# Kernel tuning notes

Measured on AMD Instinct MI355X. Metric: run time of the kernel, lower is better.

Reference implementation:

```python
import jax, jax.numpy as jnp
import numpy as np

B, T, C, DU, OUT = 16, 2048, 1024, 1024, 512
CIF_THRESHOLD = 1.0


def setup_inputs():
    key = jax.random.key(0)
    k0, k1, k2, k3, k4, k5 = jax.random.split(key, 6)
    encoder_out = jax.random.normal(k0, (B, T, C), dtype=jnp.float32)
    input_lengths = (T // 2 + jax.random.randint(k1, (B,), 0, T // 2)).astype(jnp.int32)
    target_lengths = (200 + jax.random.randint(k2, (B,), 0, 300)).astype(jnp.int32)
    s = 1.0 / np.sqrt(C)
    Wd = jax.random.uniform(k3, (DU, C), jnp.float32, -s, s)
    bd = jnp.zeros((DU,), jnp.float32)
    sp = 1.0 / np.sqrt(DU)
    Wp = jax.random.uniform(k4, (1, DU), jnp.float32, -sp, sp)
    bp = jnp.zeros((1,), jnp.float32)
    Wo = jax.random.uniform(k5, (OUT, C), jnp.float32, -s, s)
    return {"encoder_out": encoder_out, "input_lengths": input_lengths,
            "target_lengths": target_lengths, "Wd": Wd, "bd": bd,
            "Wp": Wp, "bp": bp, "Wo": Wo}


def _cif_forward(encoder_out, input_lengths, target_lengths, Wd, bd, Wp, bp, Wo):
    Bsz, Tlen, Cdim = encoder_out.shape
    pos = jnp.arange(Tlen)
    not_pad = (pos[None, :] < input_lengths[:, None]).astype(encoder_out.dtype)  # [B,T]

    # dense weight production: relu(x Wd^T + bd) -> sigmoid(. Wp^T + bp)
    h = jax.nn.relu(jnp.einsum('btc,dc->btd', encoder_out, Wd) + bd)
    weight = jax.nn.sigmoid(jnp.einsum('btd,od->bto', h, Wp)[..., 0] + bp[0])
    org_weight = weight * not_pad

    # training-time scaling so weights sum to target_lengths
    scale = target_lengths.astype(encoder_out.dtype) / (org_weight.sum(-1) + 1e-8)
    weight = org_weight * scale[:, None]

    padding_start_id = input_lengths  # = not_padding_mask.sum(-1)

    def step(carry, xs):
        acc_w, acc_s = carry                     # [B], [B,C]
        w, e, i = xs                             # [B], [B,C], scalar step idx
        fired = (acc_w + w) >= CIF_THRESHOLD     # [B]
        remained = 1.0 - acc_w
        new_w = jnp.where(fired, w - remained, w + acc_w)
        new_s = jnp.where(fired[:, None], (w - remained)[:, None] * e,
                          acc_s + w[:, None] * e)
        f_s = jnp.where(fired[:, None], acc_s + remained[:, None] * e, 0.0)
        f_s = jnp.where((i > padding_start_id)[:, None], 0.0, f_s)
        return (new_w, new_s), f_s

    init = (jnp.zeros((Bsz,), encoder_out.dtype),
            jnp.zeros((Bsz, Cdim), encoder_out.dtype))
    _, fired_states = jax.lax.scan(
        step, init,
        (weight.T, jnp.transpose(encoder_out, (1, 0, 2)), jnp.arange(Tlen)))
    fired_states = jnp.transpose(fired_states, (1, 0, 2))  # [B,T,C]

    fired_marks = jnp.abs(fired_states).sum(-1) != 0.0     # [B,T]
    # stable-compact fired frames to front; pad to T (upper bound of fired_max_length)
    order = jnp.argsort(jnp.logical_not(fired_marks).astype(jnp.int32), axis=1)
    n_fired = fired_marks.sum(-1)                           # [B]
    valid = pos[None, :] < n_fired[:, None]                 # [B,T]
    cif_outputs = jnp.take_along_axis(fired_states, order[:, :, None], axis=1)
    cif_outputs = cif_outputs * valid[:, :, None].astype(cif_outputs.dtype)

    idx = jnp.where(valid, order, 0).astype(jnp.int32)
    prev = jnp.concatenate([jnp.zeros((Bsz, 1), jnp.int32), idx[:, :-1]], axis=1)
    cif_durations = (idx - prev) * valid.astype(jnp.int32)

    base_mask = (pos[None, :] == 0).astype(jnp.int32)       # [1,0,0,...] fallback
    cif_out_padding_mask = jnp.where((n_fired > 0)[:, None],
                                     valid.astype(jnp.int32), base_mask)
    quantity_out = org_weight.sum(-1)                       # training branch
    cif_outputs = jnp.einsum('btc,oc->bto', cif_outputs, Wo)  # bias-free output proj
    return cif_outputs, cif_out_padding_mask, cif_durations, quantity_out


def reference(encoder_out, input_lengths, target_lengths, Wd, bd, Wp, bp, Wo):
    return _cif_forward(encoder_out, input_lengths, target_lengths,
                        Wd, bd, Wp, bp, Wo)
```

## Files before the change

kernel.cpp:

```cpp
#include <hip/hip_runtime.h>
#include <cstdint>
#include <cstddef>

#define BSZ 16
#define TLEN 2048
#define CDIM 1024
#define OUTDIM 512
#define MAXF 512

typedef _Float16 f16x8 __attribute__((ext_vector_type(8)));
typedef _Float16 f16x4 __attribute__((ext_vector_type(4)));
typedef float f32x16 __attribute__((ext_vector_type(16)));

__device__ __forceinline__ void gl_lds16(const void* g, void* l) {
    __builtin_amdgcn_global_load_lds(
        (const __attribute__((address_space(1))) void*)g,
        (__attribute__((address_space(3))) void*)l, 16, 0, 0);
}

struct h2pair { _Float16 h0, h1; };
__device__ __forceinline__ h2pair split2(float a) {
    h2pair o;
    o.h0 = (_Float16)a;
    float r = a - (float)o.h0;
    o.h1 = (_Float16)(r * 2048.0f);
    return o;
}

__global__ __launch_bounds__(128) void k0a_split_wd(
    const float* __restrict__ Wd, _Float16* __restrict__ B0,
    _Float16* __restrict__ B1)
{
    const int dut = blockIdx.x;
    const int ktl = blockIdx.y;
    const int r = threadIdx.x;
    const float* src = Wd + (size_t)(dut * 128 + r) * CDIM + ktl * 32;
    float v[32];
#pragma unroll
    for (int j = 0; j < 8; j++) *(float4*)&v[j * 4] = *(const float4*)(src + j * 4);
    const size_t tb = (size_t)(dut * 32 + ktl) * 4096;
#pragma unroll
    for (int c = 0; c < 4; c++) {
        f16x8 h0, h1;
#pragma unroll
        for (int j = 0; j < 8; j++) {
            h2pair s = split2(v[c * 8 + j]);
            h0[j] = s.h0;
            h1[j] = s.h1;
        }
        *(f16x8*)&B0[tb + (c * 128 + r) * 8] = h0;
        *(f16x8*)&B1[tb + (c * 128 + r) * 8] = h1;
    }
}

__global__ __launch_bounds__(256) void k0c_split_wo(
    const float* __restrict__ Wo, _Float16* __restrict__ W0,
    _Float16* __restrict__ W1)
{
    const int i = (blockIdx.x * 256 + threadIdx.x) * 4;
    float4 v = *(const float4*)(Wo + i);
    f16x4 h0, h1;
    h2pair s0 = split2(v.x); h0[0] = s0.h0; h1[0] = s0.h1;
    h2pair s1 = split2(v.y); h0[1] = s1.h0; h1[1] = s1.h1;
    h2pair s2 = split2(v.z); h0[2] = s2.h0; h1[2] = s2.h1;
    h2pair s3 = split2(v.w); h0[3] = s3.h0; h1[3] = s3.h1;
    *(f16x4*)&W0[i] = h0;
    *(f16x4*)&W1[i] = h1;
}

__global__ __launch_bounds__(256, 2) void k1_weight_gemm(
    const float* __restrict__ enc, const _Float16* __restrict__ BT0,
    const _Float16* __restrict__ BT1, const float* __restrict__ bd,
    const float* __restrict__ Wp, float* __restrict__ g)
{
    __shared__ __align__(16) _Float16 lds[32768];

    const int tid = threadIdx.x;
    const int lane = tid & 63;
    const int wv = tid >> 6;
    const int l5 = lane & 31;
    const int hi = lane >> 5;
    const int mtb = (wv & 1) * 64;
    const int ntb = (wv >> 1) * 64;

    const int bx = blockIdx.x;
    const int xcd = bx & 7;
    const int j = bx >> 3;
    const int rg = xcd * 32 + (j >> 3);
    const int du = j & 7;
    const long row0 = (long)rg * 128;
    const int du0 = du * 128;

    const int sr = tid >> 1;
    const int sh = tid & 1;
    const float* aptr = enc + (row0 + sr) * (long)CDIM + sh * 16;

    const _Float16* btile = ((wv >> 1) ? BT1 : BT0) + (size_t)du * 32 * 4096;
    const int bh = wv & 1;
    const int bofs = 8192 + (wv >> 1) * 4096 + bh * 2048;

    f32x16 acc[2][2], accc[2][2];
#pragma unroll
    for (int mt = 0; mt < 2; mt++)
#pragma unroll
        for (int nt = 0; nt < 2; nt++)
#pragma unroll
            for (int r = 0; r < 16; r++) { acc[mt][nt][r] = 0.f; accc[mt][nt][r] = 0.f; }

    float fa[16];

#pragma unroll
    for (int jj = 0; jj < 4; jj++)
        *(float4*)&fa[jj * 4] = *(const float4*)(aptr + jj * 4);
    {
        f16x8 va0[2], va1[2];
#pragma unroll
        for (int c = 0; c < 2; c++)
#pragma unroll
            for (int jj = 0; jj < 8; jj++) {
                h2pair s = split2(fa[c * 8 + jj]);
                va0[c][jj] = s.h0;
                va1[c][jj] = s.h1;
            }
#pragma unroll
        for (int c = 0; c < 2; c++) {
            *(f16x8*)&lds[((sh * 2 + c) * 128 + sr) * 8] = va0[c];
            *(f16x8*)&lds[4096 + ((sh * 2 + c) * 128 + sr) * 8] = va1[c];
        }
#pragma unroll
        for (int c = 0; c < 4; c++)
            gl_lds16(btile + (bh * 256 + c * 64 + lane) * 8,
                     &lds[bofs + c * 512]);
    }
#pragma unroll
    for (int jj = 0; jj < 4; jj++)
        *(float4*)&fa[jj * 4] = *(const float4*)(aptr + 32 + jj * 4);

    for (int kt = 0; kt < 32; ++kt) {
        const int cur = (kt & 1) * 16384;
        const int nxt = ((kt & 1) ^ 1) * 16384;

        __syncthreads();

        if (kt < 31) {
#pragma unroll
            for (int c = 0; c < 4; c++)
                gl_lds16(btile + (size_t)(kt + 1) * 4096 + (bh * 256 + c * 64 + lane) * 8,
                         &lds[nxt + bofs + c * 512]);
            f16x8 va0[2], va1[2];
#pragma unroll
            for (int c = 0; c < 2; c++)
#pragma unroll
                for (int jj = 0; jj < 8; jj++) {
                    h2pair s = split2(fa[c * 8 + jj]);
                    va0[c][jj] = s.h0;
                    va1[c][jj] = s.h1;
                }
#pragma unroll
            for (int c = 0; c < 2; c++) {
                *(f16x8*)&lds[nxt + ((sh * 2 + c) * 128 + sr) * 8] = va0[c];
                *(f16x8*)&lds[nxt + 4096 + ((sh * 2 + c) * 128 + sr) * 8] = va1[c];
            }
            if (kt < 30) {
#pragma unroll
                for (int jj = 0; jj < 4; jj++)
                    *(float4*)&fa[jj * 4] = *(const float4*)(aptr + (kt + 2) * 32 + jj * 4);
            }
        }

#pragma unroll
        for (int ks = 0; ks < 2; ks++) {
            const int ch = ks * 2 + hi;
            f16x8 A0[2], A1[2], B0[2], B1[2];
#pragma unroll
            for (int mt = 0; mt < 2; mt++) {
                const int row = mtb + mt * 32 + l5;
                A0[mt] = *(const f16x8*)&lds[cur + (ch * 128 + row) * 8];
                A1[mt] = *(const f16x8*)&lds[cur + 4096 + (ch * 128 + row) * 8];
            }
#pragma unroll
            for (int nt = 0; nt < 2; nt++) {
                const int row = ntb + nt * 32 + l5;
                B0[nt] = *(const f16x8*)&lds[cur + 8192 + (ch * 128 + row) * 8];
                B1[nt] = *(const f16x8*)&lds[cur + 12288 + (ch * 128 + row) * 8];
            }
#pragma unroll
            for (int mt = 0; mt < 2; mt++)
#pragma unroll
                for (int nt = 0; nt < 2; nt++) {
                    acc[mt][nt] = __builtin_amdgcn_mfma_f32_32x32x16_f16(
                        A0[mt], B0[nt], acc[mt][nt], 0, 0, 0);
                    accc[mt][nt] = __builtin_amdgcn_mfma_f32_32x32x16_f16(
                        A0[mt], B1[nt], accc[mt][nt], 0, 0, 0);
                    accc[mt][nt] = __builtin_amdgcn_mfma_f32_32x32x16_f16(
                        A1[mt], B0[nt], accc[mt][nt], 0, 0, 0);
                }
        }
    }

    float bdv[2], wpv[2];
#pragma unroll
    for (int nt = 0; nt < 2; nt++) {
        int n = du0 + ntb + nt * 32 + l5;
        bdv[nt] = bd[n];
        wpv[nt] = Wp[n];
    }
    float pm[2][16];
#pragma unroll
    for (int mt = 0; mt < 2; mt++)
#pragma unroll
        for (int r = 0; r < 16; r++) {
            float s = 0.f;
#pragma unroll
            for (int nt = 0; nt < 2; nt++) {
                float h = acc[mt][nt][r] + 4.8828125e-4f * accc[mt][nt][r] + bdv[nt];
                h = h > 0.f ? h : 0.f;
                s += wpv[nt] * h;
            }
            s += __shfl_xor(s, 1);
            s += __shfl_xor(s, 2);
            s += __shfl_xor(s, 4);
            s += __shfl_xor(s, 8);
            s += __shfl_xor(s, 16);
            pm[mt][r] = s;
        }
    float out = 0.f;
#pragma unroll
    for (int mt = 0; mt < 2; mt++)
#pragma unroll
        for (int r = 0; r < 16; r++)
            if (l5 == mt * 16 + r) out = pm[mt][r];
    const int mt_sel = l5 >> 4;
    const int r_sel = l5 & 15;
    const int row = mtb + mt_sel * 32 + (r_sel & 3) + 8 * (r_sel >> 2) + 4 * hi;
    atomicAdd(&g[row0 + row], out);
}

__global__ __launch_bounds__(256) void k2_scan(
    const float* __restrict__ g, const int* __restrict__ in_len,
    const int* __restrict__ tgt_len, const float* __restrict__ bp,
    float* __restrict__ c_a, float* __restrict__ c_b,
    int* __restrict__ fire_t, int* __restrict__ n_fired,
    float* __restrict__ out_mask, float* __restrict__ out_dur,
    float* __restrict__ out_qty)
{
    __shared__ float w[TLEN];
    __shared__ float ca[TLEN];
    __shared__ float cb[TLEN];
    __shared__ int fires[MAXF];
    __shared__ float ssum[256];
    __shared__ float s_scale;
    __shared__ int s_nf;

    const int b = blockIdx.x;
    const int tid = threadIdx.x;
    const int len = in_len[b];
    const float bpv = bp[0];

    float local = 0.f;
    for (int t = tid; t < TLEN; t += 256) {
        float gv = g[b * TLEN + t] + bpv;
        float s = 1.f / (1.f + expf(-gv));
        float ow = (t < len) ? s : 0.f;
        w[t] = ow;
        local += ow;
    }
    ssum[tid] = local;
    __syncthreads();
    for (int st = 128; st > 0; st >>= 1) {
        if (tid < st) ssum[tid] += ssum[tid + st];
        __syncthreads();
    }
    if (tid == 0) {
        float org_sum = ssum[0];
        out_qty[b] = org_sum;
        s_scale = (float)tgt_len[b] / (org_sum + 1e-8f);
    }
    __syncthreads();
    float scale = s_scale;
    for (int t = tid; t < TLEN; t += 256) w[t] *= scale;
    __syncthreads();

    if (tid == 0) {
        float accw = 0.f;
        int k = 0;
        int t = 0;
        for (; t + 8 <= len; t += 8) {
            float4 wa = *(const float4*)&w[t];
            float4 wb4 = *(const float4*)&w[t + 4];
            float wv8[8] = {wa.x, wa.y, wa.z, wa.w, wb4.x, wb4.y, wb4.z, wb4.w};
#pragma unroll
            for (int u = 0; u < 8; u++) {
                float wt = wv8[u];
                float aw = accw + wt;
                bool f = (aw >= 1.0f);
                float rem = 1.0f - accw;
                float fb = wt - rem;
                ca[t + u] = f ? rem : wt;
                cb[t + u] = f ? fb : 0.f;
                fires[k & (MAXF - 1)] = t + u;
                k += f ? 1 : 0;
                accw = f ? fb : aw;
            }
        }
        for (; t < len; t++) {
            float wt = w[t];
            float aw = accw + wt;
            bool f = (aw >= 1.0f);
            float rem = 1.0f - accw;
            float fb = wt - rem;
            ca[t] = f ? rem : wt;
            cb[t] = f ? fb : 0.f;
            fires[k & (MAXF - 1)] = t;
            k += f ? 1 : 0;
            accw = f ? fb : aw;
        }
        s_nf = (k < MAXF) ? k : MAXF;
        n_fired[b] = s_nf;
    }
    __syncthreads();

    for (int t = tid; t < len; t += 256) {
        c_a[b * TLEN + t] = ca[t];
        c_b[b * TLEN + t] = cb[t];
    }
    const int nf = s_nf;
    for (int jj = tid; jj < nf; jj += 256) {
        int tj = fires[jj];
        fire_t[b * MAXF + jj] = tj;
        out_mask[b * TLEN + jj] = 1.0f;
        int prev = (jj == 0) ? 0 : fires[jj - 1];
        out_dur[b * TLEN + jj] = (float)(tj - prev);
    }
    if (tid == 0 && nf == 0) out_mask[b * TLEN] = 1.0f;
}

__global__ __launch_bounds__(256) void k3a_compact(
    const float* __restrict__ enc, const float* __restrict__ c_a,
    const float* __restrict__ c_b, const int* __restrict__ fire_t,
    const int* __restrict__ n_fired, _Float16* __restrict__ C0,
    _Float16* __restrict__ C1)
{
    const int b = blockIdx.y;
    const int k = blockIdx.x;
    const int tid = threadIdx.x;
    _Float16* d0 = C0 + ((size_t)b * MAXF + k) * CDIM + tid * 4;
    _Float16* d1 = C1 + ((size_t)b * MAXF + k) * CDIM + tid * 4;
    if (k >= n_fired[b]) {
        f16x4 z = {(_Float16)0.f, (_Float16)0.f, (_Float16)0.f, (_Float16)0.f};
        *(f16x4*)d0 = z;
        *(f16x4*)d1 = z;
        return;
    }
    const int tend = fire_t[b * MAXF + k];
    const int tprev = (k == 0) ? -1 : fire_t[b * MAXF + k - 1];
    float ax = 0.f, ay = 0.f, az = 0.f, aw = 0.f;
    const int tstart = (tprev < 0) ? 0 : tprev;
    for (int t = tstart; t <= tend; t++) {
        float coef = (t == tprev) ? c_b[b * TLEN + t] : c_a[b * TLEN + t];
        const float4 e = *(const float4*)(enc + ((size_t)b * TLEN + t) * CDIM + tid * 4);
        ax += coef * e.x;
        ay += coef * e.y;
        az += coef * e.z;
        aw += coef * e.w;
    }
    f16x4 h0, h1;
    h2pair s0 = split2(ax); h0[0] = s0.h0; h1[0] = s0.h1;
    h2pair s1 = split2(ay); h0[1] = s1.h0; h1[1] = s1.h1;
    h2pair s2 = split2(az); h0[2] = s2.h0; h1[2] = s2.h1;
    h2pair s3 = split2(aw); h0[3] = s3.h0; h1[3] = s3.h1;
    *(f16x4*)d0 = h0;
    *(f16x4*)d1 = h1;
}

__global__ __launch_bounds__(256, 2) void k3b_outproj(
    const _Float16* __restrict__ C0, const _Float16* __restrict__ C1,
    const _Float16* __restrict__ W0, const _Float16* __restrict__ W1,
    const int* __restrict__ n_fired, float* __restrict__ out0)
{
    __shared__ __align__(16) _Float16 lds[16384];

    const int b = blockIdx.z;
    const int nf = n_fired[b];
    const int j0 = blockIdx.x * 128;
    if (j0 >= nf) return;
    const int o0 = blockIdx.y * 128;
    const int tid = threadIdx.x;
    const int lane = tid & 63;
    const int wv = tid >> 6;
    const int l5 = lane & 31;
    const int hi = lane >> 5;
    const int mtb = (wv & 1) * 64;
    const int ntb = (wv >> 1) * 64;

    const int sr = tid >> 1;
    const int sh = tid & 1;
    const _Float16* a0p = C0 + ((size_t)b * MAXF + j0 + sr) * CDIM + sh * 16;
    const _Float16* a1p = C1 + ((size_t)b * MAXF + j0 + sr) * CDIM + sh * 16;
    const _Float16* b0p = W0 + (size_t)(o0 + sr) * CDIM + sh * 16;
    const _Float16* b1p = W1 + (size_t)(o0 + sr) * CDIM + sh * 16;

    f32x16 acc[2][2], accc[2][2];
#pragma unroll
    for (int mt = 0; mt < 2; mt++)
#pragma unroll
        for (int nt = 0; nt < 2; nt++)
#pragma unroll
            for (int r = 0; r < 16; r++) { acc[mt][nt][r] = 0.f; accc[mt][nt][r] = 0.f; }

    f16x8 xa0[2], xa1[2], xb0[2], xb1[2];
#pragma unroll
    for (int c = 0; c < 2; c++) {
        xa0[c] = *(const f16x8*)(a0p + c * 8);
        xa1[c] = *(const f16x8*)(a1p + c * 8);
        xb0[c] = *(const f16x8*)(b0p + c * 8);
        xb1[c] = *(const f16x8*)(b1p + c * 8);
    }

    for (int kt = 0; kt < 32; ++kt) {
        __syncthreads();
#pragma unroll
        for (int c = 0; c < 2; c++) {
            *(f16x8*)&lds[((sh * 2 + c) * 128 + sr) * 8] = xa0[c];
            *(f16x8*)&lds[4096 + ((sh * 2 + c) * 128 + sr) * 8] = xa1[c];
            *(f16x8*)&lds[8192 + ((sh * 2 + c) * 128 + sr) * 8] = xb0[c];
            *(f16x8*)&lds[12288 + ((sh * 2 + c) * 128 + sr) * 8] = xb1[c];
        }
        __syncthreads();
        if (kt < 31) {
            const int o = (kt + 1) * 32;
#pragma unroll
            for (int c = 0; c < 2; c++) {
                xa0[c] = *(const f16x8*)(a0p + o + c * 8);
                xa1[c] = *(const f16x8*)(a1p + o + c * 8);
                xb0[c] = *(const f16x8*)(b0p + o + c * 8);
                xb1[c] = *(const f16x8*)(b1p + o + c * 8);
            }
        }
#pragma unroll
        for (int ks = 0; ks < 2; ks++) {
            const int ch = ks * 2 + hi;
            f16x8 A0[2], A1[2], B0[2], B1[2];
#pragma unroll
            for (int mt = 0; mt < 2; mt++) {
                const int row = mtb + mt * 32 + l5;
                A0[mt] = *(const f16x8*)&lds[(ch * 128 + row) * 8];
                A1[mt] = *(const f16x8*)&lds[4096 + (ch * 128 + row) * 8];
            }
#pragma unroll
            for (int nt = 0; nt < 2; nt++) {
                const int row = ntb + nt * 32 + l5;
                B0[nt] = *(const f16x8*)&lds[8192 + (ch * 128 + row) * 8];
                B1[nt] = *(const f16x8*)&lds[12288 + (ch * 128 + row) * 8];
            }
#pragma unroll
            for (int mt = 0; mt < 2; mt++)
#pragma unroll
                for (int nt = 0; nt < 2; nt++) {
                    acc[mt][nt] = __builtin_amdgcn_mfma_f32_32x32x16_f16(
                        A0[mt], B0[nt], acc[mt][nt], 0, 0, 0);
                    accc[mt][nt] = __builtin_amdgcn_mfma_f32_32x32x16_f16(
                        A0[mt], B1[nt], accc[mt][nt], 0, 0, 0);
                    accc[mt][nt] = __builtin_amdgcn_mfma_f32_32x32x16_f16(
                        A1[mt], B0[nt], accc[mt][nt], 0, 0, 0);
                }
        }
    }

#pragma unroll
    for (int mt = 0; mt < 2; mt++)
#pragma unroll
        for (int nt = 0; nt < 2; nt++)
#pragma unroll
            for (int r = 0; r < 16; r++) {
                float val = acc[mt][nt][r] + 4.8828125e-4f * accc[mt][nt][r];
                int m = mtb + mt * 32 + (r & 3) + 8 * (r >> 2) + 4 * hi;
                int col = o0 + ntb + nt * 32 + l5;
                out0[((size_t)b * TLEN + j0 + m) * OUTDIM + col] = val;
            }
}

extern "C" void kernel_launch(void* const* d_in, const int* in_sizes, int n_in,
                              void* d_out, int out_size, void* d_ws, size_t ws_size,
                              hipStream_t stream)
{
    const float* enc = (const float*)d_in[0];
    const int* in_len = (const int*)d_in[1];
    const int* tgt_len = (const int*)d_in[2];
    const float* Wd = (const float*)d_in[3];
    const float* bd = (const float*)d_in[4];
    const float* Wp = (const float*)d_in[5];
    const float* bp = (const float*)d_in[6];
    const float* Wo = (const float*)d_in[7];

    char* ws = (char*)d_ws;
    float* g       = (float*)(ws + 0);
    float* c_a     = (float*)(ws + 131072);
    float* c_b     = (float*)(ws + 262144);
    int* fire_t    = (int*)(ws + 393216);
    int* n_fired   = (int*)(ws + 425984);
    _Float16* WdT0 = (_Float16*)(ws + 458752);
    _Float16* WdT1 = (_Float16*)(ws + 2555904);
    _Float16* Wo0  = (_Float16*)(ws + 4653056);
    _Float16* Wo1  = (_Float16*)(ws + 5701632);
    _Float16* C0   = (_Float16*)(ws + 6750208);
    _Float16* C1   = (_Float16*)(ws + 23527424);

    float* out0 = (float*)d_out;
    float* out_mask = out0 + (size_t)BSZ * TLEN * OUTDIM;
    float* out_dur = out_mask + (size_t)BSZ * TLEN;
    float* out_qty = out_dur + (size_t)BSZ * TLEN;

    (void)hipMemsetAsync(g, 0, 131072, stream);
    (void)hipMemsetAsync(d_out, 0, (size_t)out_size * 4, stream);

    k0a_split_wd<<<dim3(8, 32), 128, 0, stream>>>(Wd, WdT0, WdT1);
    k0c_split_wo<<<512, 256, 0, stream>>>(Wo, Wo0, Wo1);
    k1_weight_gemm<<<2048, 256, 0, stream>>>(enc, WdT0, WdT1, bd, Wp, g);
    k2_scan<<<BSZ, 256, 0, stream>>>(g, in_len, tgt_len, bp, c_a, c_b,
                                     fire_t, n_fired, out_mask, out_dur, out_qty);
    k3a_compact<<<dim3(MAXF, BSZ), 256, 0, stream>>>(enc, c_a, c_b, fire_t,
                                                     n_fired, C0, C1);
    k3b_outproj<<<dim3(4, 4, BSZ), 256, 0, stream>>>(C0, C1, Wo0, Wo1,
                                                     n_fired, out0);
}
```

Baseline: 591.6 us.

## Interleave A-tile split/store between MFMA halves with manual waitcnt barriers

Restructures the main K loop of the dense-weight GEMM. The fp32-to-split-fp16 conversion and LDS store of the next A tile now sit between the two k-substep MFMA groups, so VALU and LDS work overlaps matrix math. The __syncthreads at loop top is replaced by one end-of-iteration s_barrier preceded by explicit s_waitcnt vmcnt(4)/lgkmcnt(0), which lets the next iteration's A prefetch global loads stay in flight. s_setprio raises wave priority around MFMA blocks. The hand-written waitcnt counts depend on exact instruction ordering and could race if the compiler reorders loads.

```diff
diff --git a/kernel.cpp b/kernel.cpp
--- a/kernel.cpp
+++ b/kernel.cpp
@@ -132,45 +132,27 @@
             gl_lds16(btile + (bh * 256 + c * 64 + lane) * 8,
                      &lds[bofs + c * 512]);
     }
+    asm volatile("" ::: "memory");
 #pragma unroll
     for (int jj = 0; jj < 4; jj++)
         *(float4*)&fa[jj * 4] = *(const float4*)(aptr + 32 + jj * 4);
+    asm volatile("s_waitcnt vmcnt(4) lgkmcnt(0)" ::: "memory");
+    __builtin_amdgcn_s_barrier();
 
     for (int kt = 0; kt < 32; ++kt) {
         const int cur = (kt & 1) * 16384;
-        const int nxt = ((kt & 1) ^ 1) * 16384;
-
-        __syncthreads();
+        const int nxt = cur ^ 16384;
 
         if (kt < 31) {
 #pragma unroll
             for (int c = 0; c < 4; c++)
                 gl_lds16(btile + (size_t)(kt + 1) * 4096 + (bh * 256 + c * 64 + lane) * 8,
                          &lds[nxt + bofs + c * 512]);
-            f16x8 va0[2], va1[2];
-#pragma unroll
-            for (int c = 0; c < 2; c++)
-#pragma unroll
-                for (int jj = 0; jj < 8; jj++) {
-                    h2pair s = split2(fa[c * 8 + jj]);
-                    va0[c][jj] = s.h0;
-                    va1[c][jj] = s.h1;
-                }
-#pragma unroll
-            for (int c = 0; c < 2; c++) {
-                *(f16x8*)&lds[nxt + ((sh * 2 + c) * 128 + sr) * 8] = va0[c];
-                *(f16x8*)&lds[nxt + 4096 + ((sh * 2 + c) * 128 + sr) * 8] = va1[c];
-            }
-            if (kt < 30) {
-#pragma unroll
-                for (int jj = 0; jj < 4; jj++)
-                    *(float4*)&fa[jj * 4] = *(const float4*)(aptr + (kt + 2) * 32 + jj * 4);
-            }
-        }
-
-#pragma unroll
-        for (int ks = 0; ks < 2; ks++) {
-            const int ch = ks * 2 + hi;
+        }
+        asm volatile("" ::: "memory");
+
+        {
+            const int ch = hi;
             f16x8 A0[2], A1[2], B0[2], B1[2];
 #pragma unroll
             for (int mt = 0; mt < 2; mt++) {
@@ -184,6 +166,7 @@
                 B0[nt] = *(const f16x8*)&lds[cur + 8192 + (ch * 128 + row) * 8];
                 B1[nt] = *(const f16x8*)&lds[cur + 12288 + (ch * 128 + row) * 8];
             }
+            __builtin_amdgcn_s_setprio(1);
 #pragma unroll
             for (int mt = 0; mt < 2; mt++)
 #pragma unroll
@@ -195,6 +178,70 @@
                     accc[mt][nt] = __builtin_amdgcn_mfma_f32_32x32x16_f16(
                         A1[mt], B0[nt], accc[mt][nt], 0, 0, 0);
                 }
+            __builtin_amdgcn_s_setprio(0);
+        }
+
+        f16x8 A0b[2], A1b[2], B0b[2], B1b[2];
+        {
+            const int ch = 2 + hi;
+#pragma unroll
+            for (int mt = 0; mt < 2; mt++) {
+                const int row = mtb + mt * 32 + l5;
+                A0b[mt] = *(const f16x8*)&lds[cur + (ch * 128 + row) * 8];
+                A1b[mt] = *(const f16x8*)&lds[cur + 4096 + (ch * 128 + row) * 8];
+            }
+#pragma unroll
+            for (int nt = 0; nt < 2; nt++) {
+                const int row = ntb + nt * 32 + l5;
+                B0b[nt] = *(const f16x8*)&lds[cur + 8192 + (ch * 128 + row) * 8];
+                B1b[nt] = *(const f16x8*)&lds[cur + 12288 + (ch * 128 + row) * 8];
+            }
+        }
+
+        if (kt < 31) {
+            f16x8 va0[2], va1[2];
+#pragma unroll
+            for (int c = 0; c < 2; c++)
+#pragma unroll
+                for (int jj = 0; jj < 8; jj++) {
+                    h2pair s = split2(fa[c * 8 + jj]);
+                    va0[c][jj] = s.h0;
+                    va1[c][jj] = s.h1;
+                }
+#pragma unroll
+            for (int c = 0; c < 2; c++) {
+                *(f16x8*)&lds[nxt + ((sh * 2 + c) * 128 + sr) * 8] = va0[c];
+                *(f16x8*)&lds[nxt + 4096 + ((sh * 2 + c) * 128 + sr) * 8] = va1[c];
+            }
+            if (kt < 30) {
+#pragma unroll
+                for (int jj = 0; jj < 4; jj++)
+                    *(float4*)&fa[jj * 4] = *(const float4*)(aptr + (kt + 2) * 32 + jj * 4);
+            }
+        }
+
+        {
+            __builtin_amdgcn_s_setprio(1);
+#pragma unroll
+            for (int mt = 0; mt < 2; mt++)
+#pragma unroll
+                for (int nt = 0; nt < 2; nt++) {
+                    acc[mt][nt] = __builtin_amdgcn_mfma_f32_32x32x16_f16(
+                        A0b[mt], B0b[nt], acc[mt][nt], 0, 0, 0);
+                    accc[mt][nt] = __builtin_amdgcn_mfma_f32_32x32x16_f16(
+                        A0b[mt], B1b[nt], accc[mt][nt], 0, 0, 0);
+                    accc[mt][nt] = __builtin_amdgcn_mfma_f32_32x32x16_f16(
+                        A1b[mt], B0b[nt], accc[mt][nt], 0, 0, 0);
+                }
+            __builtin_amdgcn_s_setprio(0);
+        }
+
+        if (kt < 31) {
+            if (kt < 30)
+                asm volatile("s_waitcnt vmcnt(4) lgkmcnt(0)" ::: "memory");
+            else
+                asm volatile("s_waitcnt vmcnt(0) lgkmcnt(0)" ::: "memory");
+            __builtin_amdgcn_s_barrier();
         }
     }
 
```

Measured after the change: 605.0 us. 2.3% more time.

## Pre-split encoder into fp16 tiles and stream both operands via async LDS loads

Applied to the files above, without the earlier changes.

Adds a separate pass that splits the fp32 encoder into hi/lo fp16 tiled buffers. The weight GEMM then loads both A and B tiles with global_load_lds instead of converting A in registers each k-step. The block grows to 512 threads (8 waves, 32-wide N per wave) and MFMA sections are wrapped in setprio. This removes per-iteration split work and register staging from the GEMM loop, but adds a full extra read/write pass over the 128MB encoder (writing 128MB of fp16 halves), which may cost more than it saves. E0 reuses the C0 workspace region, which relies on ordering with later kernels.

```diff
diff --git a/kernel.cpp b/kernel.cpp
--- a/kernel.cpp
+++ b/kernel.cpp
@@ -27,18 +27,18 @@
     return o;
 }
 
-__global__ __launch_bounds__(128) void k0a_split_wd(
-    const float* __restrict__ Wd, _Float16* __restrict__ B0,
-    _Float16* __restrict__ B1)
-{
-    const int dut = blockIdx.x;
+__global__ __launch_bounds__(128) void k0_split_tiled(
+    const float* __restrict__ src_, _Float16* __restrict__ P0,
+    _Float16* __restrict__ P1)
+{
+    const int rgp = blockIdx.x;
     const int ktl = blockIdx.y;
     const int r = threadIdx.x;
-    const float* src = Wd + (size_t)(dut * 128 + r) * CDIM + ktl * 32;
+    const float* src = src_ + (size_t)(rgp * 128 + r) * CDIM + ktl * 32;
     float v[32];
 #pragma unroll
     for (int j = 0; j < 8; j++) *(float4*)&v[j * 4] = *(const float4*)(src + j * 4);
-    const size_t tb = (size_t)(dut * 32 + ktl) * 4096;
+    const size_t tb = (size_t)(rgp * 32 + ktl) * 4096;
 #pragma unroll
     for (int c = 0; c < 4; c++) {
         f16x8 h0, h1;
@@ -48,8 +48,8 @@
             h0[j] = s.h0;
             h1[j] = s.h1;
         }
-        *(f16x8*)&B0[tb + (c * 128 + r) * 8] = h0;
-        *(f16x8*)&B1[tb + (c * 128 + r) * 8] = h1;
+        *(f16x8*)&P0[tb + (c * 128 + r) * 8] = h0;
+        *(f16x8*)&P1[tb + (c * 128 + r) * 8] = h1;
     }
 }
 
@@ -68,10 +68,11 @@
     *(f16x4*)&W1[i] = h1;
 }
 
-__global__ __launch_bounds__(256, 2) void k1_weight_gemm(
-    const float* __restrict__ enc, const _Float16* __restrict__ BT0,
-    const _Float16* __restrict__ BT1, const float* __restrict__ bd,
-    const float* __restrict__ Wp, float* __restrict__ g)
+__global__ __launch_bounds__(512, 4) void k1_weight_gemm(
+    const _Float16* __restrict__ E0, const _Float16* __restrict__ E1,
+    const _Float16* __restrict__ BT0, const _Float16* __restrict__ BT1,
+    const float* __restrict__ bd, const float* __restrict__ Wp,
+    float* __restrict__ g)
 {
     __shared__ __align__(16) _Float16 lds[32768];
 
@@ -80,143 +81,98 @@
     const int wv = tid >> 6;
     const int l5 = lane & 31;
     const int hi = lane >> 5;
-    const int mtb = (wv & 1) * 64;
-    const int ntb = (wv >> 1) * 64;
+    const int wm = wv & 1;
+    const int wn = wv >> 1;
+    const int mtb = wm * 64;
+    const int ntb = wn * 32;
 
     const int bx = blockIdx.x;
     const int xcd = bx & 7;
     const int j = bx >> 3;
     const int rg = xcd * 32 + (j >> 3);
-    const int du = j & 7;
+    const int dug = j & 7;
     const long row0 = (long)rg * 128;
-    const int du0 = du * 128;
-
-    const int sr = tid >> 1;
-    const int sh = tid & 1;
-    const float* aptr = enc + (row0 + sr) * (long)CDIM + sh * 16;
-
-    const _Float16* btile = ((wv >> 1) ? BT1 : BT0) + (size_t)du * 32 * 4096;
-    const int bh = wv & 1;
-    const int bofs = 8192 + (wv >> 1) * 4096 + bh * 2048;
-
-    f32x16 acc[2][2], accc[2][2];
+    const int du0 = dug * 128;
+
+    const int region = wv >> 1;
+    const int halfsel = wv & 1;
+    const _Float16* srcbase =
+        (region == 0) ? E0 : (region == 1) ? E1 : (region == 2) ? BT0 : BT1;
+    const size_t tb = (region < 2) ? (size_t)(rg * 32) * 4096
+                                   : (size_t)(dug * 32) * 4096;
+    const int ldsreg = region * 4096;
+    const int cbase = halfsel * 4;
+
+    f32x16 acc[2], accc[2];
 #pragma unroll
     for (int mt = 0; mt < 2; mt++)
 #pragma unroll
-        for (int nt = 0; nt < 2; nt++)
-#pragma unroll
-            for (int r = 0; r < 16; r++) { acc[mt][nt][r] = 0.f; accc[mt][nt][r] = 0.f; }
-
-    float fa[16];
-
-#pragma unroll
-    for (int jj = 0; jj < 4; jj++)
-        *(float4*)&fa[jj * 4] = *(const float4*)(aptr + jj * 4);
-    {
-        f16x8 va0[2], va1[2];
-#pragma unroll
-        for (int c = 0; c < 2; c++)
-#pragma unroll
-            for (int jj = 0; jj < 8; jj++) {
-                h2pair s = split2(fa[c * 8 + jj]);
-                va0[c][jj] = s.h0;
-                va1[c][jj] = s.h1;
-            }
-#pragma unroll
-        for (int c = 0; c < 2; c++) {
-            *(f16x8*)&lds[((sh * 2 + c) * 128 + sr) * 8] = va0[c];
-            *(f16x8*)&lds[4096 + ((sh * 2 + c) * 128 + sr) * 8] = va1[c];
-        }
-#pragma unroll
-        for (int c = 0; c < 4; c++)
-            gl_lds16(btile + (bh * 256 + c * 64 + lane) * 8,
-                     &lds[bofs + c * 512]);
-    }
-#pragma unroll
-    for (int jj = 0; jj < 4; jj++)
-        *(float4*)&fa[jj * 4] = *(const float4*)(aptr + 32 + jj * 4);
+        for (int r = 0; r < 16; r++) { acc[mt][r] = 0.f; accc[mt][r] = 0.f; }
+
+#pragma unroll
+    for (int c = 0; c < 4; c++)
+        gl_lds16(srcbase + tb + (cbase + c) * 512 + lane * 8,
+                 &lds[ldsreg + (cbase + c) * 512]);
+    asm volatile("s_waitcnt vmcnt(0)" ::: "memory");
+    __builtin_amdgcn_s_barrier();
 
     for (int kt = 0; kt < 32; ++kt) {
         const int cur = (kt & 1) * 16384;
-        const int nxt = ((kt & 1) ^ 1) * 16384;
-
-        __syncthreads();
+        const int nxt = cur ^ 16384;
 
         if (kt < 31) {
+            const size_t tbk = tb + (size_t)(kt + 1) * 4096;
 #pragma unroll
             for (int c = 0; c < 4; c++)
-                gl_lds16(btile + (size_t)(kt + 1) * 4096 + (bh * 256 + c * 64 + lane) * 8,
-                         &lds[nxt + bofs + c * 512]);
-            f16x8 va0[2], va1[2];
-#pragma unroll
-            for (int c = 0; c < 2; c++)
-#pragma unroll
-                for (int jj = 0; jj < 8; jj++) {
-                    h2pair s = split2(fa[c * 8 + jj]);
-                    va0[c][jj] = s.h0;
-                    va1[c][jj] = s.h1;
-                }
-#pragma unroll
-            for (int c = 0; c < 2; c++) {
-                *(f16x8*)&lds[nxt + ((sh * 2 + c) * 128 + sr) * 8] = va0[c];
-                *(f16x8*)&lds[nxt + 4096 + ((sh * 2 + c) * 128 + sr) * 8] = va1[c];
-            }
-            if (kt < 30) {
-#pragma unroll
-                for (int jj = 0; jj < 4; jj++)
-                    *(float4*)&fa[jj * 4] = *(const float4*)(aptr + (kt + 2) * 32 + jj * 4);
-            }
-        }
-
-#pragma unroll
-        for (int ks = 0; ks < 2; ks++) {
-            const int ch = ks * 2 + hi;
-            f16x8 A0[2], A1[2], B0[2], B1[2];
+                gl_lds16(srcbase + tbk + (cbase + c) * 512 + lane * 8,
+                         &lds[nxt + ldsreg + (cbase + c) * 512]);
+        }
+        asm volatile("" ::: "memory");
+
+#pragma unroll
+        for (int p = 0; p < 2; p++) {
+            const int cq = p * 2 + hi;
+            f16x8 A0[2], A1[2], B0, B1;
 #pragma unroll
             for (int mt = 0; mt < 2; mt++) {
                 const int row = mtb + mt * 32 + l5;
-                A0[mt] = *(const f16x8*)&lds[cur + (ch * 128 + row) * 8];
-                A1[mt] = *(const f16x8*)&lds[cur + 4096 + (ch * 128 + row) * 8];
-            }
-#pragma unroll
-            for (int nt = 0; nt < 2; nt++) {
-                const int row = ntb + nt * 32 + l5;
-                B0[nt] = *(const f16x8*)&lds[cur + 8192 + (ch * 128 + row) * 8];
-                B1[nt] = *(const f16x8*)&lds[cur + 12288 + (ch * 128 + row) * 8];
-            }
-#pragma unroll
-            for (int mt = 0; mt < 2; mt++)
-#pragma unroll
-                for (int nt = 0; nt < 2; nt++) {
-                    acc[mt][nt] = __builtin_amdgcn_mfma_f32_32x32x16_f16(
-                        A0[mt], B0[nt], acc[mt][nt], 0, 0, 0);
-                    accc[mt][nt] = __builtin_amdgcn_mfma_f32_32x32x16_f16(
-                        A0[mt], B1[nt], accc[mt][nt], 0, 0, 0);
-                    accc[mt][nt] = __builtin_amdgcn_mfma_f32_32x32x16_f16(
-                        A1[mt], B0[nt], accc[mt][nt], 0, 0, 0);
-                }
-        }
-    }
-
-    float bdv[2], wpv[2];
-#pragma unroll
-    for (int nt = 0; nt < 2; nt++) {
-        int n = du0 + ntb + nt * 32 + l5;
-        bdv[nt] = bd[n];
-        wpv[nt] = Wp[n];
-    }
+                A0[mt] = *(const f16x8*)&lds[cur + (cq * 128 + row) * 8];
+                A1[mt] = *(const f16x8*)&lds[cur + 4096 + (cq * 128 + row) * 8];
+            }
+            {
+                const int row = ntb + l5;
+                B0 = *(const f16x8*)&lds[cur + 8192 + (cq * 128 + row) * 8];
+                B1 = *(const f16x8*)&lds[cur + 12288 + (cq * 128 + row) * 8];
+            }
+            __builtin_amdgcn_s_setprio(1);
+#pragma unroll
+            for (int mt = 0; mt < 2; mt++) {
+                acc[mt] = __builtin_amdgcn_mfma_f32_32x32x16_f16(
+                    A0[mt], B0, acc[mt], 0, 0, 0);
+                accc[mt] = __builtin_amdgcn_mfma_f32_32x32x16_f16(
+                    A0[mt], B1, accc[mt], 0, 0, 0);
+                accc[mt] = __builtin_amdgcn_mfma_f32_32x32x16_f16(
+                    A1[mt], B0, accc[mt], 0, 0, 0);
+            }
+            __builtin_amdgcn_s_setprio(0);
+        }
+
+        if (kt < 31) {
+            asm volatile("s_waitcnt vmcnt(0) lgkmcnt(0)" ::: "memory");
+            __builtin_amdgcn_s_barrier();
+        }
+    }
+
+    const float bdv = bd[du0 + ntb + l5];
+    const float wpv = Wp[du0 + ntb + l5];
     float pm[2][16];
 #pragma unroll
     for (int mt = 0; mt < 2; mt++)
 #pragma unroll
         for (int r = 0; r < 16; r++) {
-            float s = 0.f;
-#pragma unroll
-            for (int nt = 0; nt < 2; nt++) {
-                float h = acc[mt][nt][r] + 4.8828125e-4f * accc[mt][nt][r] + bdv[nt];
-                h = h > 0.f ? h : 0.f;
-                s += wpv[nt] * h;
-            }
+            float h = acc[mt][r] + 4.8828125e-4f * accc[mt][r] + bdv;
+            h = h > 0.f ? h : 0.f;
+            float s = wpv * h;
             s += __shfl_xor(s, 1);
             s += __shfl_xor(s, 2);
             s += __shfl_xor(s, 4);
@@ -505,6 +461,8 @@
     _Float16* Wo1  = (_Float16*)(ws + 5701632);
     _Float16* C0   = (_Float16*)(ws + 6750208);
     _Float16* C1   = (_Float16*)(ws + 23527424);
+    _Float16* E0   = (_Float16*)(ws + 6750208);
+    _Float16* E1   = (_Float16*)(ws + 73859072);
 
     float* out0 = (float*)d_out;
     float* out_mask = out0 + (size_t)BSZ * TLEN * OUTDIM;
@@ -514,9 +472,10 @@
     (void)hipMemsetAsync(g, 0, 131072, stream);
     (void)hipMemsetAsync(d_out, 0, (size_t)out_size * 4, stream);
 
-    k0a_split_wd<<<dim3(8, 32), 128, 0, stream>>>(Wd, WdT0, WdT1);
+    k0_split_tiled<<<dim3(8, 32), 128, 0, stream>>>(Wd, WdT0, WdT1);
+    k0_split_tiled<<<dim3(256, 32), 128, 0, stream>>>(enc, E0, E1);
     k0c_split_wo<<<512, 256, 0, stream>>>(Wo, Wo0, Wo1);
-    k1_weight_gemm<<<2048, 256, 0, stream>>>(enc, WdT0, WdT1, bd, Wp, g);
+    k1_weight_gemm<<<2048, 512, 0, stream>>>(E0, E1, WdT0, WdT1, bd, Wp, g);
     k2_scan<<<BSZ, 256, 0, stream>>>(g, in_len, tgt_len, bp, c_a, c_b,
                                      fire_t, n_fired, out_mask, out_dur, out_qty);
     k3a_compact<<<dim3(MAXF, BSZ), 256, 0, stream>>>(enc, c_a, c_b, fire_t,
```

Result: slower. 652.6 us (+10.3%).
